# Kernel optimization log

Measured on AMD Instinct MI355X. Metric: run time of the kernel, lower is better.

## Reference

```python
import jax, jax.numpy as jnp
import numpy as np

B, S, D = 2, 2048, 1024
H, DK = 16, 64          # n_heads, head dim
HI, DI = 4, 64          # indexer heads, indexer dim
TOP_K = 512
ROPE_BASE = 10000.0


def _rope(x):
    # x: [B, S, H, DK]  (torchtune-style interleaved rotary)
    half = DK // 2
    theta = 1.0 / (ROPE_BASE ** (jnp.arange(0, DK, 2, dtype=jnp.float32) / DK))  # [half]
    ang = jnp.arange(S, dtype=jnp.float32)[:, None] * theta[None, :]             # [S, half]
    cos = jnp.cos(ang)[None, :, None, :].astype(x.dtype)                          # [1,S,1,half]
    sin = jnp.sin(ang)[None, :, None, :].astype(x.dtype)
    xs = x.reshape(x.shape[:-1] + (half, 2))
    x1, x2 = xs[..., 0], xs[..., 1]
    out = jnp.stack([x1 * cos - x2 * sin, x2 * cos + x1 * sin], axis=-1)
    return out.reshape(x.shape)


def setup_inputs() -> dict:
    key = jax.random.key(0)
    ks = jax.random.split(key, 6)
    std = 0.02
    return {
        "x": jax.random.normal(ks[0], (B, S, D), dtype=jnp.float32),
        "Wqkv": jax.random.normal(ks[1], (D, 3 * D), dtype=jnp.float32) * std,
        "Wo": jax.random.normal(ks[2], (D, D), dtype=jnp.float32) * std,
        "Wq_idx": jax.random.normal(ks[3], (D, HI * DI), dtype=jnp.float32) * std,
        "Wk_idx": jax.random.normal(ks[4], (D, DI), dtype=jnp.float32) * std,
        "Ww_idx": jax.random.normal(ks[5], (D, HI), dtype=jnp.float32) * std,
    }


def reference(x, Wqkv, Wo, Wq_idx, Wk_idx, Ww_idx):
    # ---- main QKV + RoPE ----
    qkv = (x @ Wqkv).reshape(B, S, 3, H, DK)
    q, k, v = qkv[:, :, 0], qkv[:, :, 1], qkv[:, :, 2]  # [B,S,H,DK]
    q = _rope(q)
    k = _rope(k)
    Q = q.transpose(0, 2, 1, 3)  # [B,H,S,DK]
    K = k.transpose(0, 2, 1, 3)
    V = v.transpose(0, 2, 1, 3)

    # ---- lightning indexer: I[b,t,s] = sum_h w[b,t,h] * relu(q_i . k_i) ----
    qi = (x @ Wq_idx).reshape(B, S, HI, DI)
    ki = x @ Wk_idx                              # [B,S,DI]
    w = x @ Ww_idx                               # [B,S,HI]
    dots = jnp.einsum("bthd,bsd->bths", qi, ki)  # [B,S,HI,S]
    index_scores = jnp.einsum("bths,bth->bts", jax.nn.relu(dots), w)

    # ---- top-k token selection (causal penalty of -1e9, as in original) ----
    causal = jnp.triu(jnp.ones((S, S), dtype=bool), k=1)
    masked_scores = jnp.where(causal[None], -1e9, index_scores)
    _, top_idx = jax.lax.top_k(masked_scores, TOP_K)  # [B,S,TOP_K]
    b_idx = jnp.arange(B)[:, None, None]
    t_idx = jnp.arange(S)[None, :, None]
    sel_mask = jnp.zeros((B, S, S), dtype=bool).at[b_idx, t_idx, top_idx].set(True)

    # ---- masked SDPA over full S^2 (additive mask, replicating original) ----
    add_mask = jnp.where(sel_mask[:, None], 0.0, -jnp.inf).astype(Q.dtype)  # [B,1,S,S]
    logits = jnp.einsum("bhtd,bhsd->bhts", Q, K) / jnp.sqrt(jnp.float32(DK)).astype(Q.dtype)
    probs = jax.nn.softmax(logits + add_mask, axis=-1)
    attn = jnp.einsum("bhts,bhsd->bhtd", probs, V)       # [B,H,S,DK]
    attn = attn.transpose(0, 2, 1, 3).reshape(B, S, D)
    return attn @ Wo
```

## Files before the change

kernel.cpp:

```cpp
#include <hip/hip_runtime.h>
#include <hip/hip_fp16.h>
#include <hip/hip_bf16.h>
#include <math.h>

#define BB 2
#define SS 2048
#define HH 16
#define TOPK 512
#define ROWS (BB*SS)
#define KDIM 1024
#define KP 3072
#define NSTR 384

using bf16x8 = __attribute__((ext_vector_type(8))) short;
using f32x4  = __attribute__((ext_vector_type(4))) float;
typedef _Float16 f16x8 __attribute__((ext_vector_type(8)));
typedef unsigned int u32;

__device__ __forceinline__ void gload16(const void* g, void* l) {
  __builtin_amdgcn_global_load_lds(
      (const __attribute__((address_space(1))) u32*)g,
      (__attribute__((address_space(3))) u32*)l, 16, 0, 0);
}

__device__ __forceinline__ void split_bf16(float f, short& hi, short& lo) {
  __hip_bfloat16 h = __float2bfloat16(f);
  float fh = __bfloat162float(h);
  __hip_bfloat16 l = __float2bfloat16(f - fh);
  hi = *reinterpret_cast<short*>(&h);
  lo = *reinterpret_cast<short*>(&l);
}

__device__ __forceinline__ unsigned fkey(float f) {
  unsigned u = __float_as_uint(f);
  if ((u << 1) == 0u) u = 0u;
  return (u & 0x80000000u) ? ~u : (u | 0x80000000u);
}

__global__ void rope_tab_k(float* __restrict__ ct, float* __restrict__ st) {
  int idx = blockIdx.x * blockDim.x + threadIdx.x;
  if (idx >= SS * 32) return;
  int s = idx >> 5, j = idx & 31;
  float theta = 1.0f / powf(10000.0f, (float)(2 * j) / 64.0f);
  float ang = (float)s * theta;
  float sv, cv;
  sincosf(ang, &sv, &cv);
  ct[idx] = cv;
  st[idx] = sv;
}

__global__ __launch_bounds__(256) void pack_a_k(
    const float* __restrict__ X, short* __restrict__ A, int total4)
{
  int idx = blockIdx.x * 256 + threadIdx.x;
  if (idx >= total4) return;
  float4 v = ((const float4*)X)[idx];
  float a4[4] = {v.x, v.y, v.z, v.w};
  short o[12];
#pragma unroll
  for (int j = 0; j < 4; ++j) {
    short hs, ls; split_bf16(a4[j], hs, ls);
    o[3*j] = hs; o[3*j+1] = hs; o[3*j+2] = ls;
  }
  short* op = A + (size_t)idx * 12;
  *(short4*)(op)     = *(short4*)&o[0];
  *(short4*)(op + 4) = *(short4*)&o[4];
  *(short4*)(op + 8) = *(short4*)&o[8];
}

__global__ __launch_bounds__(256) void pack_bt_k(
    const float* __restrict__ W, short* __restrict__ BT, int Nw)
{
  __shared__ float tile[32][33];
  int kb = blockIdx.y * 32, nb = blockIdx.x * 32;
  int tx = threadIdx.x & 31, ty = threadIdx.x >> 5;
  for (int yy = ty; yy < 32; yy += 8) {
    float v = 0.f;
    if (nb + tx < Nw) v = W[(size_t)(kb + yy) * Nw + nb + tx];
    tile[yy][tx] = v;
  }
  __syncthreads();
  for (int yy = ty; yy < 32; yy += 8) {
    int n = nb + yy;
    if (n >= Nw) continue;
    int k = kb + tx;
    float f = tile[tx][yy];
    short hs, ls; split_bf16(f, hs, ls);
    short* orow = BT + (size_t)n * KP + 3 * k;
    orow[0] = hs; orow[1] = ls; orow[2] = hs;
  }
}

__global__ __launch_bounds__(256) void pack_wcat_k(
    const float* __restrict__ Wq, const float* __restrict__ Wk,
    const float* __restrict__ Ww, float* __restrict__ Wcat)
{
  int idx = blockIdx.x * 256 + threadIdx.x;
  if (idx >= 1024 * NSTR) return;
  int k = idx / NSTR, n = idx - k * NSTR;
  float v = 0.f;
  if (n < 256)      v = Wq[(size_t)k * 256 + n];
  else if (n < 320) v = Wk[(size_t)k * 64 + (n - 256)];
  else if (n < 324) v = Ww[(size_t)k * 4 + (n - 320)];
  Wcat[idx] = v;
}

__global__ __launch_bounds__(256) void gemm_bf16(
    const short* __restrict__ A, const short* __restrict__ BT,
    float* __restrict__ C, int M, int N, int Kp)
{
  __shared__ short As[128 * 64];
  __shared__ short Bs[128 * 64];
  const int tid = threadIdx.x;
  const int lane = tid & 63;
  const int wv = tid >> 6;
  const int m0 = blockIdx.y * 128, n0 = blockIdx.x * 128;
  const int wr = (wv >> 1) * 64, wc = (wv & 1) * 64;
  f32x4 acc[4][4];
#pragma unroll
  for (int i = 0; i < 4; ++i)
#pragma unroll
    for (int j = 0; j < 4; ++j)
#pragma unroll
      for (int r = 0; r < 4; ++r) acc[i][j][r] = 0.0f;

  const int rsel = lane & 15;
  const int lrow = lane >> 3;
  const int lcol = (lane & 7) * 8;
  for (int k0 = 0; k0 < Kp; k0 += 64) {
#pragma unroll
    for (int q = 0; q < 4; ++q) {
      int c = wv * 4 + q;
      int row = c * 8 + lrow;
      gload16(A  + (size_t)(m0 + row) * Kp + k0 + lcol, &As[c * 512]);
      gload16(BT + (size_t)(n0 + row) * Kp + k0 + lcol, &Bs[c * 512]);
    }
    __syncthreads();
#pragma unroll
    for (int kk = 0; kk < 2; ++kk) {
      bf16x8 af[4], bfr[4];
      int kof = kk * 32 + (lane >> 4) * 8;
#pragma unroll
      for (int i = 0; i < 4; ++i) {
        af[i]  = *(const bf16x8*)&As[(wr + i * 16 + rsel) * 64 + kof];
        bfr[i] = *(const bf16x8*)&Bs[(wc + i * 16 + rsel) * 64 + kof];
      }
#pragma unroll
      for (int i = 0; i < 4; ++i)
#pragma unroll
        for (int j = 0; j < 4; ++j)
          acc[i][j] = __builtin_amdgcn_mfma_f32_16x16x32_bf16(af[i], bfr[j], acc[i][j], 0, 0, 0);
    }
    __syncthreads();
  }
  const int er = m0 + wr + (lane >> 4) * 4;
  const int ec = n0 + wc + rsel;
#pragma unroll
  for (int i = 0; i < 4; ++i)
#pragma unroll
    for (int j = 0; j < 4; ++j)
#pragma unroll
      for (int r = 0; r < 4; ++r)
        C[(size_t)(er + i * 16 + r) * N + ec + j * 16] = acc[i][j][r];
}

__global__ __launch_bounds__(128) void gemm_idx_k(
    const float* __restrict__ A, const float* __restrict__ Bw, float* __restrict__ C)
{
  __shared__ float As[16][36];
  __shared__ float Bs[16][68];
  int n0 = blockIdx.x * 64, m0 = blockIdx.y * 32;
  int tid = threadIdx.x;
  int tr = tid >> 4;
  int tc = tid & 15;
  float acc[4][4];
#pragma unroll
  for (int i = 0; i < 4; ++i)
#pragma unroll
    for (int j = 0; j < 4; ++j) acc[i][j] = 0.f;

  for (int k0 = 0; k0 < 1024; k0 += 16) {
    {
      int lin = tid * 4;
      int row = lin >> 4, kk = lin & 15;
      float4 av = *(const float4*)(A + (size_t)(m0 + row) * 1024 + k0 + kk);
      As[kk + 0][row] = av.x; As[kk + 1][row] = av.y;
      As[kk + 2][row] = av.z; As[kk + 3][row] = av.w;
      int lin2 = tid * 8;
      int bk = lin2 >> 6, bc = lin2 & 63;
      const float* bp = Bw + (size_t)(k0 + bk) * NSTR + n0 + bc;
      *(float4*)&Bs[bk][bc]     = *(const float4*)(bp);
      *(float4*)&Bs[bk][bc + 4] = *(const float4*)(bp + 4);
    }
    __syncthreads();
#pragma unroll
    for (int k = 0; k < 16; ++k) {
      float a[4], b[4];
      *(float4*)&a[0] = *(const float4*)&As[k][tr * 4];
      *(float4*)&b[0] = *(const float4*)&Bs[k][tc * 4];
#pragma unroll
      for (int i = 0; i < 4; ++i)
#pragma unroll
        for (int j = 0; j < 4; ++j)
          acc[i][j] = fmaf(a[i], b[j], acc[i][j]);
    }
    __syncthreads();
  }
#pragma unroll
  for (int i = 0; i < 4; ++i)
    *(float4*)(C + (size_t)(m0 + tr * 4 + i) * NSTR + n0 + tc * 4) = *(float4*)&acc[i][0];
}

__global__ __launch_bounds__(256) void qkv_post_k(
    const float* __restrict__ C, const float* __restrict__ ct, const float* __restrict__ st,
    __half* __restrict__ Qh, __half* __restrict__ Kh, __half* __restrict__ Vh)
{
  int idx = blockIdx.x * 256 + threadIdx.x;
  if (idx >= ROWS * 384) return;
  int m = idx / 384;
  int g = idx - m * 384;
  int col0 = g * 8;
  const float* cp = C + (size_t)m * 3072 + col0;
  float4 v0 = *(const float4*)cp;
  float4 v1 = *(const float4*)(cp + 4);
  float a[8] = {v0.x, v0.y, v0.z, v0.w, v1.x, v1.y, v1.z, v1.w};
  int sec = col0 >> 10;
  int cin = col0 & 1023;
  size_t orow = (size_t)m * 1024 + cin;
  if (sec == 2) {
    __half2 hh[4];
#pragma unroll
    for (int c = 0; c < 4; ++c) hh[c] = __floats2half2_rn(a[2*c], a[2*c+1]);
    *(float4*)(Vh + orow) = *(float4*)hh;
  } else {
    int t = m & (SS - 1);
    int jb = (cin & 63) >> 1;
    float o[8];
#pragma unroll
    for (int c = 0; c < 4; ++c) {
      float cv = ct[t * 32 + jb + c], sv = st[t * 32 + jb + c];
      float x1 = a[2*c], x2 = a[2*c+1];
      o[2*c]   = x1 * cv - x2 * sv;
      o[2*c+1] = x2 * cv + x1 * sv;
    }
    if (sec == 0) {
#pragma unroll
      for (int c = 0; c < 8; ++c) o[c] *= 0.125f;
    }
    __half2 hh[4];
#pragma unroll
    for (int c = 0; c < 4; ++c) hh[c] = __floats2half2_rn(o[2*c], o[2*c+1]);
    __half* dst = (sec == 0) ? Qh : Kh;
    *(float4*)(dst + orow) = *(float4*)hh;
  }
}

__global__ __launch_bounds__(256) void vt_k(
    const __half* __restrict__ Vh, __half* __restrict__ VhT)
{
  int st = blockIdx.x, bh = blockIdx.y;
  int b = bh >> 4, h = bh & 15;
  int s0 = st * 64;
  __shared__ __half tile[64][65];
  int tid = threadIdx.x;
#pragma unroll
  for (int rnd = 0; rnd < 2; ++rnd) {
    int row = (tid >> 3) + rnd * 32;
    int c8 = (tid & 7) * 8;
    *(float4*)&tile[row][c8] =
        *(const float4*)(Vh + ((size_t)b * SS + s0 + row) * 1024 + h * 64 + c8);
  }
  __syncthreads();
#pragma unroll
  for (int rnd = 0; rnd < 2; ++rnd) {
    int d = (tid >> 3) + rnd * 32;
    int s8 = (tid & 7) * 8;
    __half tmp[8];
#pragma unroll
    for (int j = 0; j < 8; ++j) tmp[j] = tile[s8 + j][d];
    *(float4*)(VhT + ((size_t)bh * 64 + d) * 2048 + s0 + s8) = *(float4*)tmp;
  }
}

__global__ __launch_bounds__(256) void idx_topk_k(
    const float* __restrict__ Ccat, u32* __restrict__ msk)
{
  int t = blockIdx.x, b = blockIdx.y;
  int tid = threadIdx.x;
  int lane = tid & 63;
  int wv = tid >> 6;
  if (t < TOPK) {
    if (tid < 64)
      msk[((size_t)b * SS + t) * 64 + tid] = (tid < 16) ? 0xFFFFFFFFu : 0u;
    return;
  }
  __shared__ u32 uk[SS];
  __shared__ u32 hist[256];
  __shared__ u32 w[64];
  __shared__ u32 s_bsel, s_above;

  if (tid < 64) w[tid] = 0u;

  const float4* qrow = (const float4*)(Ccat + ((size_t)b * SS + t) * NSTR);
  const float* wrow = Ccat + ((size_t)b * SS + t) * NSTR + 320;
  float w0 = wrow[0], w1 = wrow[1], w2 = wrow[2], w3 = wrow[3];

#pragma unroll 1
  for (int s0 = 0; s0 <= t; s0 += 256) {
    int s = s0 + tid;
    if (s <= t) {
      const float4* kp = (const float4*)(Ccat + ((size_t)b * SS + s) * NSTR + 256);
      float a0 = 0.f, a1 = 0.f, a2 = 0.f, a3 = 0.f;
#pragma unroll
      for (int d4 = 0; d4 < 16; ++d4) {
        float4 kv = kp[d4];
        float4 q0 = qrow[d4];
        float4 q1 = qrow[16 + d4];
        float4 q2 = qrow[32 + d4];
        float4 q3 = qrow[48 + d4];
        a0 += q0.x * kv.x + q0.y * kv.y + q0.z * kv.z + q0.w * kv.w;
        a1 += q1.x * kv.x + q1.y * kv.y + q1.z * kv.z + q1.w * kv.w;
        a2 += q2.x * kv.x + q2.y * kv.y + q2.z * kv.z + q2.w * kv.w;
        a3 += q3.x * kv.x + q3.y * kv.y + q3.z * kv.z + q3.w * kv.w;
      }
      float v = fmaxf(a0, 0.f) * w0 + fmaxf(a1, 0.f) * w1 +
                fmaxf(a2, 0.f) * w2 + fmaxf(a3, 0.f) * w3;
      uk[s] = fkey(v);
    }
  }

  unsigned krem = TOPK;
  unsigned prefix = 0;
#pragma unroll 1
  for (int p = 0; p < 4; ++p) {
    int shift = 24 - 8 * p;
    u32 maskAbove = (p == 0) ? 0u : (0xFFFFFFFFu << (shift + 8));
    hist[tid] = 0u;
    __syncthreads();
#pragma unroll 1
    for (int s0 = 0; s0 <= t; s0 += 256) {
      int s = s0 + tid;
      if (s <= t) {
        u32 key = uk[s];
        if ((key & maskAbove) == prefix)
          atomicAdd(&hist[(key >> shift) & 255], 1u);
      }
    }
    __syncthreads();
    if (wv == 0) {
      uint4 hv = *(uint4*)&hist[lane * 4];
      u32 lsum = hv.x + hv.y + hv.z + hv.w;
      u32 x = lsum;
#pragma unroll
      for (int off = 1; off < 64; off <<= 1) {
        u32 y = __shfl_down(x, off);
        x += (lane + off < 64) ? y : 0u;
      }
      u32 esuf = x - lsum;
      u32 S3 = esuf + hv.w;
      u32 S2 = S3 + hv.z;
      u32 S1 = S2 + hv.y;
      u32 S0 = S1 + hv.x;
      if (S0 >= krem && S1 < krem)  { s_bsel = lane * 4 + 0; s_above = S1; }
      if (S1 >= krem && S2 < krem)  { s_bsel = lane * 4 + 1; s_above = S2; }
      if (S2 >= krem && S3 < krem)  { s_bsel = lane * 4 + 2; s_above = S3; }
      if (S3 >= krem && esuf < krem){ s_bsel = lane * 4 + 3; s_above = esuf; }
    }
    __syncthreads();
    prefix |= (s_bsel << shift);
    krem -= s_above;
  }

  u32 Tkey = prefix;
  unsigned kfin = krem;

#pragma unroll 1
  for (int s0 = 0; s0 <= t; s0 += 256) {
    int s = s0 + tid;
    bool pred = (s <= t) && (uk[s] > Tkey);
    unsigned long long mba = __ballot(pred);
    int wbase = (s0 + wv * 64) >> 5;
    if (lane == 0 && (u32)mba) atomicOr(&w[wbase], (u32)mba);
    if (lane == 32 && (u32)(mba >> 32)) atomicOr(&w[wbase + 1], (u32)(mba >> 32));
  }
  if (wv == 0) {
    unsigned taken = 0;
#pragma unroll 1
    for (int s0 = 0; s0 <= t && taken < kfin; s0 += 64) {
      int s = s0 + lane;
      bool pred = (s <= t) && (uk[s] == Tkey);
      unsigned long long mba = __ballot(pred);
      unsigned pre = (unsigned)__popcll(mba & ((1ull << lane) - 1ull));
      if (pred && (taken + pre) < kfin)
        atomicOr(&w[s >> 5], 1u << (s & 31));
      taken += (unsigned)__popcll(mba);
    }
  }
  __syncthreads();
  if (tid < 64) msk[((size_t)b * SS + t) * 64 + tid] = w[tid];
}

__global__ __launch_bounds__(256) void attn_dense_k(
    const __half* __restrict__ Qh, const __half* __restrict__ Kh,
    const __half* __restrict__ VhT, const u32* __restrict__ msk,
    float* __restrict__ attnO)
{
  int bid = blockIdx.x;
  int xcd = bid & 7, loc = bid >> 3;
  int bh = xcd * 4 + (loc >> 5);
  int qt = loc & 31;
  int b = bh >> 4, h = bh & 15;
  int t0 = qt * 64;

  const int tid = threadIdx.x;
  const int lane = tid & 63;
  const int wv = tid >> 6;
  const int l15 = lane & 15;
  const int g = lane >> 4;

  __shared__ short lds[12800];
  short* Ks = lds;
  short* Vt = lds + 4096;
  short* Ps = lds + 8192 + wv * 1088;
  u32* mlds = (u32*)(lds + 12544);

  const size_t brow = (size_t)b * SS;

  f16x8 qf0, qf1;
  {
    const __half* qp = Qh + (brow + t0 + wv * 16 + l15) * 1024 + h * 64 + g * 8;
    qf0 = *(const f16x8*)(qp);
    qf1 = *(const f16x8*)(qp + 32);
  }

  f32x4 accO[4];
#pragma unroll
  for (int n2 = 0; n2 < 4; ++n2)
#pragma unroll
    for (int r = 0; r < 4; ++r) accO[n2][r] = 0.f;
  float mRun[4] = {-1e30f, -1e30f, -1e30f, -1e30f};
  float sRun[4] = {0.f, 0.f, 0.f, 0.f};

  const int srow = lane >> 3;
  const int scp  = (lane & 7) ^ srow;

#pragma unroll 1
  for (int kt = 0; kt < 32; ++kt) {
    int kt0 = kt * 64;
#pragma unroll
    for (int q = 0; q < 2; ++q) {
      int j = wv * 2 + q;
      gload16(Kh + (brow + kt0 + j * 8 + srow) * 1024 + h * 64 + scp * 8, Ks + j * 512);
      gload16(VhT + ((size_t)(bh * 64 + j * 8 + srow)) * 2048 + kt0 + scp * 8, Vt + j * 512);
    }
    if (tid < 128)
      mlds[tid] = msk[(brow + t0 + (tid >> 1)) * 64 + kt * 2 + (tid & 1)];
    __syncthreads();

    f32x4 s4[4];
#pragma unroll
    for (int ns = 0; ns < 4; ++ns) {
#pragma unroll
      for (int r = 0; r < 4; ++r) s4[ns][r] = 0.f;
      int rowk = ns * 16 + l15;
      int cp0 = g ^ (rowk & 7);
      int cp1 = (4 + g) ^ (rowk & 7);
      f16x8 kf0 = *(const f16x8*)&Ks[rowk * 64 + cp0 * 8];
      f16x8 kf1 = *(const f16x8*)&Ks[rowk * 64 + cp1 * 8];
      s4[ns] = __builtin_amdgcn_mfma_f32_16x16x32_f16(qf0, kf0, s4[ns], 0, 0, 0);
      s4[ns] = __builtin_amdgcn_mfma_f32_16x16x32_f16(qf1, kf1, s4[ns], 0, 0, 0);
    }

#pragma unroll
    for (int r = 0; r < 4; ++r) {
      int qb2 = (wv * 16 + g * 4 + r) * 2;
      u32 w0 = mlds[qb2];
      u32 w1 = mlds[qb2 + 1];
      float le[4];
#pragma unroll
      for (int ns = 0; ns < 4; ++ns) {
        u32 w = (ns < 2) ? w0 : w1;
        int bit = (ns & 1) * 16 + l15;
        float l = s4[ns][r];
        le[ns] = ((w >> bit) & 1u) ? l : -1e30f;
      }
      float cm = fmaxf(fmaxf(le[0], le[1]), fmaxf(le[2], le[3]));
      cm = fmaxf(cm, __shfl_xor(cm, 1));
      cm = fmaxf(cm, __shfl_xor(cm, 2));
      cm = fmaxf(cm, __shfl_xor(cm, 4));
      cm = fmaxf(cm, __shfl_xor(cm, 8));
      float mn = fmaxf(mRun[r], cm);
      float fac = __expf(mRun[r] - mn);
      mRun[r] = mn;
      float sum = 0.f;
#pragma unroll
      for (int ns = 0; ns < 4; ++ns) {
        float ee = __expf(le[ns] - mn);
        ee = (le[ns] < -1e29f) ? 0.f : ee;
        sum += ee;
        Ps[(g * 4 + r) * 68 + ns * 16 + l15] =
            (short)__half_as_ushort(__float2half_rn(ee));
      }
      sum += __shfl_xor(sum, 1);
      sum += __shfl_xor(sum, 2);
      sum += __shfl_xor(sum, 4);
      sum += __shfl_xor(sum, 8);
      sRun[r] = sRun[r] * fac + sum;
#pragma unroll
      for (int n2 = 0; n2 < 4; ++n2) accO[n2][r] *= fac;
    }

    f16x8 pa0, pa1;
    {
      const short* pp = &Ps[l15 * 68 + g * 8];
      float2 lo0 = *(const float2*)(pp);
      float2 hi0 = *(const float2*)(pp + 4);
      float2 lo1 = *(const float2*)(pp + 32);
      float2 hi1 = *(const float2*)(pp + 36);
      float4 c0 = make_float4(lo0.x, lo0.y, hi0.x, hi0.y);
      float4 c1 = make_float4(lo1.x, lo1.y, hi1.x, hi1.y);
      pa0 = *(const f16x8*)&c0;
      pa1 = *(const f16x8*)&c1;
    }
#pragma unroll
    for (int n2 = 0; n2 < 4; ++n2) {
      int rowd = n2 * 16 + l15;
      int cp0 = g ^ (rowd & 7);
      int cp1 = (4 + g) ^ (rowd & 7);
      f16x8 vf0 = *(const f16x8*)&Vt[rowd * 64 + cp0 * 8];
      f16x8 vf1 = *(const f16x8*)&Vt[rowd * 64 + cp1 * 8];
      accO[n2] = __builtin_amdgcn_mfma_f32_16x16x32_f16(pa0, vf0, accO[n2], 0, 0, 0);
      accO[n2] = __builtin_amdgcn_mfma_f32_16x16x32_f16(pa1, vf1, accO[n2], 0, 0, 0);
    }
    __syncthreads();
  }

#pragma unroll
  for (int r = 0; r < 4; ++r) {
    float inv = 1.0f / sRun[r];
    size_t orow = (brow + t0 + wv * 16 + g * 4 + r) * (size_t)1024 + h * 64;
#pragma unroll
    for (int n2 = 0; n2 < 4; ++n2)
      attnO[orow + n2 * 16 + l15] = accO[n2][r] * inv;
  }
}

extern "C" void kernel_launch(void* const* d_in, const int* in_sizes, int n_in,
                              void* d_out, int out_size, void* d_ws, size_t ws_size,
                              hipStream_t stream) {
  const float* x    = (const float*)d_in[0];
  const float* Wqkv = (const float*)d_in[1];
  const float* Wo   = (const float*)d_in[2];
  const float* Wq   = (const float*)d_in[3];
  const float* Wk   = (const float*)d_in[4];
  const float* Ww   = (const float*)d_in[5];
  float* out = (float*)d_out;

  float* fws = (float*)d_ws;
  size_t o = 0;
  __half* Qh    = (__half*)(fws + o);  o += (size_t)ROWS * 512;
  __half* Kh    = (__half*)(fws + o);  o += (size_t)ROWS * 512;
  __half* Vh    = (__half*)(fws + o);  o += (size_t)ROWS * 512;
  float*  ct    = fws + o;             o += (size_t)SS * 32;
  float*  st    = fws + o;             o += (size_t)SS * 32;
  float*  Ccat  = fws + o;             o += (size_t)ROWS * NSTR;
  short*  BTwo  = (short*)(fws + o);   o += (size_t)1024 * KP / 2;
  short*  BTq   = (short*)(fws + o);   o += (size_t)3072 * KP / 2;
  short*  Ax    = (short*)(fws + o);
  float*  attnO = fws + o;
  float*  Wcat  = fws + o + (size_t)ROWS * 1024;
                      o += (size_t)ROWS * KP / 2;
  float*  Cbuf  = fws + o;
  short*  Aattn = (short*)(fws + o);
  __half* VhT   = (__half*)(fws + o + (size_t)8 * 1024 * 1024);
  u32*    msk   = (u32*)(fws + o + (size_t)10500 * 1024);
  o += (size_t)ROWS * 3072;

  rope_tab_k<<<dim3((SS * 32 + 255) / 256), dim3(256), 0, stream>>>(ct, st);

  pack_a_k<<<dim3(ROWS * KDIM / 4 / 256), dim3(256), 0, stream>>>(x, Ax, ROWS * KDIM / 4);
  pack_bt_k<<<dim3(3072 / 32, 32), dim3(256), 0, stream>>>(Wqkv, BTq, 3072);
  pack_bt_k<<<dim3(1024 / 32, 32), dim3(256), 0, stream>>>(Wo, BTwo, 1024);

  gemm_bf16<<<dim3(3072 / 128, ROWS / 128), dim3(256), 0, stream>>>(
      Ax, BTq, Cbuf, ROWS, 3072, KP);
  qkv_post_k<<<dim3((ROWS * 384 + 255) / 256), dim3(256), 0, stream>>>(Cbuf, ct, st, Qh, Kh, Vh);
  vt_k<<<dim3(SS / 64, BB * HH), dim3(256), 0, stream>>>(Vh, VhT);

  pack_wcat_k<<<dim3((1024 * NSTR + 255) / 256), dim3(256), 0, stream>>>(Wq, Wk, Ww, Wcat);
  gemm_idx_k<<<dim3(NSTR / 64, ROWS / 32), dim3(128), 0, stream>>>(x, Wcat, Ccat);

  idx_topk_k<<<dim3(SS, BB), dim3(256), 0, stream>>>(Ccat, msk);
  attn_dense_k<<<dim3(1024), dim3(256), 0, stream>>>(Qh, Kh, VhT, msk, attnO);

  pack_a_k<<<dim3(ROWS * KDIM / 4 / 256), dim3(256), 0, stream>>>(attnO, Aattn, ROWS * KDIM / 4);
  gemm_bf16<<<dim3(1024 / 128, ROWS / 128), dim3(256), 0, stream>>>(
      Aattn, BTwo, out, ROWS, 1024, KP);
}
```

Measured before the change: 575.7 us.

## Split-K the projection GEMMs with fp16 partials and fuse attention output packing

Both bf16 GEMMs now split the K dimension across blockIdx.z: two slices for QKV and three for the output projection. Each slice writes fp16 partials, which the QKV post kernel and a new reduction kernel sum. The attention kernel now writes the split-bf16 A operand directly, so the separate fp32 attnO buffer and its pack kernel are gone. The goal is more blocks for the small output GEMM (64 blocks before) and less fp32 traffic. In exchange, partials are stored at fp16 precision, there is an extra reduction pass, and output partials reuse the Q/K/V buffers.

```diff
diff --git a/kernel.cpp b/kernel.cpp
--- a/kernel.cpp
+++ b/kernel.cpp
@@ -105,9 +105,9 @@
   Wcat[idx] = v;
 }
 
-__global__ __launch_bounds__(256) void gemm_bf16(
+__global__ __launch_bounds__(256) void gemm_bf16h(
     const short* __restrict__ A, const short* __restrict__ BT,
-    float* __restrict__ C, int M, int N, int Kp)
+    __half* __restrict__ C, int M, int N, int Kp, int kLen)
 {
   __shared__ short As[128 * 64];
   __shared__ short Bs[128 * 64];
@@ -115,6 +115,9 @@
   const int lane = tid & 63;
   const int wv = tid >> 6;
   const int m0 = blockIdx.y * 128, n0 = blockIdx.x * 128;
+  const int z = blockIdx.z;
+  const int kBeg = z * kLen;
+  __half* Cp = C + (size_t)z * M * N;
   const int wr = (wv >> 1) * 64, wc = (wv & 1) * 64;
   f32x4 acc[4][4];
 #pragma unroll
@@ -127,7 +130,7 @@
   const int rsel = lane & 15;
   const int lrow = lane >> 3;
   const int lcol = (lane & 7) * 8;
-  for (int k0 = 0; k0 < Kp; k0 += 64) {
+  for (int k0 = kBeg; k0 < kBeg + kLen; k0 += 64) {
 #pragma unroll
     for (int q = 0; q < 4; ++q) {
       int c = wv * 4 + q;
@@ -161,7 +164,7 @@
     for (int j = 0; j < 4; ++j)
 #pragma unroll
       for (int r = 0; r < 4; ++r)
-        C[(size_t)(er + i * 16 + r) * N + ec + j * 16] = acc[i][j][r];
+        Cp[(size_t)(er + i * 16 + r) * N + ec + j * 16] = __float2half_rn(acc[i][j][r]);
 }
 
 __global__ __launch_bounds__(128) void gemm_idx_k(
@@ -212,7 +215,7 @@
 }
 
 __global__ __launch_bounds__(256) void qkv_post_k(
-    const float* __restrict__ C, const float* __restrict__ ct, const float* __restrict__ st,
+    const __half* __restrict__ P, const float* __restrict__ ct, const float* __restrict__ st,
     __half* __restrict__ Qh, __half* __restrict__ Kh, __half* __restrict__ Vh)
 {
   int idx = blockIdx.x * 256 + threadIdx.x;
@@ -220,10 +223,20 @@
   int m = idx / 384;
   int g = idx - m * 384;
   int col0 = g * 8;
-  const float* cp = C + (size_t)m * 3072 + col0;
-  float4 v0 = *(const float4*)cp;
-  float4 v1 = *(const float4*)(cp + 4);
-  float a[8] = {v0.x, v0.y, v0.z, v0.w, v1.x, v1.y, v1.z, v1.w};
+  const __half* c0 = P + (size_t)m * 3072 + col0;
+  const __half* c1 = c0 + (size_t)ROWS * 3072;
+  float4 u = *(const float4*)c0;
+  float4 v = *(const float4*)c1;
+  const __half2* hu = (const __half2*)&u;
+  const __half2* hv = (const __half2*)&v;
+  float a[8];
+#pragma unroll
+  for (int c = 0; c < 4; ++c) {
+    float2 x = __half22float2(hu[c]);
+    float2 y = __half22float2(hv[c]);
+    a[2*c]   = x.x + y.x;
+    a[2*c+1] = x.y + y.y;
+  }
   int sec = col0 >> 10;
   int cin = col0 & 1023;
   size_t orow = (size_t)m * 1024 + cin;
@@ -403,7 +416,7 @@
 __global__ __launch_bounds__(256) void attn_dense_k(
     const __half* __restrict__ Qh, const __half* __restrict__ Kh,
     const __half* __restrict__ VhT, const u32* __restrict__ msk,
-    float* __restrict__ attnO)
+    short* __restrict__ Aattn)
 {
   int bid = blockIdx.x;
   int xcd = bid & 7, loc = bid >> 3;
@@ -538,11 +551,43 @@
 #pragma unroll
   for (int r = 0; r < 4; ++r) {
     float inv = 1.0f / sRun[r];
-    size_t orow = (brow + t0 + wv * 16 + g * 4 + r) * (size_t)1024 + h * 64;
-#pragma unroll
-    for (int n2 = 0; n2 < 4; ++n2)
-      attnO[orow + n2 * 16 + l15] = accO[n2][r] * inv;
-  }
+    size_t grow = brow + t0 + wv * 16 + g * 4 + r;
+    short* arow = Aattn + grow * 3072;
+#pragma unroll
+    for (int n2 = 0; n2 < 4; ++n2) {
+      int col = h * 64 + n2 * 16 + l15;
+      float v = accO[n2][r] * inv;
+      short hs, ls; split_bf16(v, hs, ls);
+      short* ap = arow + 3 * col;
+      ap[0] = hs; ap[1] = hs; ap[2] = ls;
+    }
+  }
+}
+
+__global__ __launch_bounds__(256) void redout_k(
+    const __half* __restrict__ O, float* __restrict__ out)
+{
+  int idx = blockIdx.x * 256 + threadIdx.x;
+  if (idx >= ROWS * 1024 / 8) return;
+  const size_t PS = (size_t)ROWS * 1024;
+  float4 u0 = *((const float4*)O + idx);
+  float4 u1 = *((const float4*)(O + PS) + idx);
+  float4 u2 = *((const float4*)(O + 2 * PS) + idx);
+  const __half2* h0 = (const __half2*)&u0;
+  const __half2* h1 = (const __half2*)&u1;
+  const __half2* h2 = (const __half2*)&u2;
+  float o[8];
+#pragma unroll
+  for (int c = 0; c < 4; ++c) {
+    float2 a = __half22float2(h0[c]);
+    float2 b = __half22float2(h1[c]);
+    float2 d = __half22float2(h2[c]);
+    o[2*c]   = a.x + b.x + d.x;
+    o[2*c+1] = a.y + b.y + d.y;
+  }
+  float* op = out + (size_t)idx * 8;
+  *(float4*)(op)     = make_float4(o[0], o[1], o[2], o[3]);
+  *(float4*)(op + 4) = make_float4(o[4], o[5], o[6], o[7]);
 }
 
 extern "C" void kernel_launch(void* const* d_in, const int* in_sizes, int n_in,
@@ -567,14 +612,14 @@
   short*  BTwo  = (short*)(fws + o);   o += (size_t)1024 * KP / 2;
   short*  BTq   = (short*)(fws + o);   o += (size_t)3072 * KP / 2;
   short*  Ax    = (short*)(fws + o);
-  float*  attnO = fws + o;
   float*  Wcat  = fws + o + (size_t)ROWS * 1024;
                       o += (size_t)ROWS * KP / 2;
-  float*  Cbuf  = fws + o;
+  __half* Ph    = (__half*)(fws + o);
   short*  Aattn = (short*)(fws + o);
   __half* VhT   = (__half*)(fws + o + (size_t)8 * 1024 * 1024);
   u32*    msk   = (u32*)(fws + o + (size_t)10500 * 1024);
   o += (size_t)ROWS * 3072;
+  __half* Oparts = (__half*)Qh;
 
   rope_tab_k<<<dim3((SS * 32 + 255) / 256), dim3(256), 0, stream>>>(ct, st);
 
@@ -582,18 +627,18 @@
   pack_bt_k<<<dim3(3072 / 32, 32), dim3(256), 0, stream>>>(Wqkv, BTq, 3072);
   pack_bt_k<<<dim3(1024 / 32, 32), dim3(256), 0, stream>>>(Wo, BTwo, 1024);
 
-  gemm_bf16<<<dim3(3072 / 128, ROWS / 128), dim3(256), 0, stream>>>(
-      Ax, BTq, Cbuf, ROWS, 3072, KP);
-  qkv_post_k<<<dim3((ROWS * 384 + 255) / 256), dim3(256), 0, stream>>>(Cbuf, ct, st, Qh, Kh, Vh);
+  gemm_bf16h<<<dim3(3072 / 128, ROWS / 128, 2), dim3(256), 0, stream>>>(
+      Ax, BTq, Ph, ROWS, 3072, KP, KP / 2);
+  qkv_post_k<<<dim3((ROWS * 384 + 255) / 256), dim3(256), 0, stream>>>(Ph, ct, st, Qh, Kh, Vh);
   vt_k<<<dim3(SS / 64, BB * HH), dim3(256), 0, stream>>>(Vh, VhT);
 
   pack_wcat_k<<<dim3((1024 * NSTR + 255) / 256), dim3(256), 0, stream>>>(Wq, Wk, Ww, Wcat);
   gemm_idx_k<<<dim3(NSTR / 64, ROWS / 32), dim3(128), 0, stream>>>(x, Wcat, Ccat);
 
   idx_topk_k<<<dim3(SS, BB), dim3(256), 0, stream>>>(Ccat, msk);
-  attn_dense_k<<<dim3(1024), dim3(256), 0, stream>>>(Qh, Kh, VhT, msk, attnO);
-
-  pack_a_k<<<dim3(ROWS * KDIM / 4 / 256), dim3(256), 0, stream>>>(attnO, Aattn, ROWS * KDIM / 4);
-  gemm_bf16<<<dim3(1024 / 128, ROWS / 128), dim3(256), 0, stream>>>(
-      Aattn, BTwo, out, ROWS, 1024, KP);
-}
+  attn_dense_k<<<dim3(1024), dim3(256), 0, stream>>>(Qh, Kh, VhT, msk, Aattn);
+
+  gemm_bf16h<<<dim3(1024 / 128, ROWS / 128, 3), dim3(256), 0, stream>>>(
+      Aattn, BTwo, Oparts, ROWS, 1024, KP, KP / 3);
+  redout_k<<<dim3(ROWS * 1024 / 8 / 256), dim3(256), 0, stream>>>(Oparts, out);
+}
```

Result: faster. 537.6 us (-6.6%).
